# Kernel tuning notes

Hardware: AMD Instinct MI355X
Metric: run time of the kernel (lower is better)

Reference implementation:

```python
import jax, jax.numpy as jnp
import numpy as np

B = 262144
SPACE = 64
H1, H2 = 128, 64
ACTION_SCALES = np.array([32, 64, 96, 128, 160, 192, 224, 256, 16, 48, 80, 112, 144, 176, 208, 240], dtype=np.int32)
MAX_SCALE = int(ACTION_SCALES.max())  # 256


def setup_inputs() -> dict:
    key = jax.random.key(0)
    ks = jax.random.split(key, 8)
    state = jax.random.normal(ks[0], (B, SPACE), dtype=jnp.float32)
    dim_idx = jax.random.randint(ks[1], (B,), 0, len(ACTION_SCALES)).astype(jnp.float32)
    # last column carries the integer dimension index, as in the torch module
    inp = jnp.concatenate([state, dim_idx[:, None]], axis=1)  # (B, SPACE+1)
    s = 1.0 / np.sqrt(SPACE + 1)
    W1 = jax.random.uniform(ks[2], (H1, SPACE + 1), jnp.float32, -s, s)
    b1 = jnp.zeros((H1,), jnp.float32)
    s = 1.0 / np.sqrt(H1)
    W2 = jax.random.uniform(ks[3], (H2, H1), jnp.float32, -s, s)
    b2 = jnp.zeros((H2,), jnp.float32)
    s = 1.0 / np.sqrt(H2)
    W3 = jax.random.uniform(ks[4], (MAX_SCALE, H2), jnp.float32, -s, s)
    b3 = jnp.zeros((MAX_SCALE,), jnp.float32)
    scale_table = jnp.asarray(ACTION_SCALES)
    return {"input": inp, "scale_table": scale_table,
            "W1": W1, "b1": b1, "W2": W2, "b2": b2, "W3": W3, "b3": b3}


def reference(input, scale_table, W1, b1, W2, b2, W3, b3):
    dim_idx = input[:, -1].astype(jnp.int32)                 # (B,)
    x = jax.nn.relu(input @ W1.T + b1)                        # (B, 128)
    x = jax.nn.relu(x @ W2.T + b2)                            # (B, 64)
    logits = x @ W3.T + b3                                    # (B, max_scale)
    scales = scale_table[dim_idx]                             # (B,) gather replaces python loop
    mask = jnp.arange(logits.shape[-1])[None, :] < scales[:, None]  # (B, max_scale) bool
    logits = jnp.where(mask, logits, jnp.float32(-1e9))
    probs = jax.nn.softmax(logits, axis=-1)
    return probs, mask
```

## Files before the change

### kernel.cpp

```cpp
#include <hip/hip_runtime.h>
#include <hip/hip_bf16.h>

#define B_ROWS 262144
#define IN_DIM 65

typedef short short8 __attribute__((ext_vector_type(8)));
typedef float f32x4 __attribute__((ext_vector_type(4)));

static __device__ __forceinline__ short f2bf(float f) {
    union { float f; unsigned u; } v; v.f = f;
    unsigned r = v.u + 0x7fff + ((v.u >> 16) & 1);
    return (short)(r >> 16);
}
static __device__ __forceinline__ float bfbits2f(unsigned hi16) {
    union { unsigned u; float f; } v; v.u = hi16;
    return v.f;
}

__global__ void convert_weights(const float* __restrict__ W1,
                                const float* __restrict__ W2,
                                const float* __restrict__ W3,
                                short* __restrict__ ws) {
    int tid = blockIdx.x * 256 + threadIdx.x;
    if (tid < 8192) {
        int n = tid >> 6, k = tid & 63;
        ws[tid] = f2bf(W1[n * IN_DIM + k]);
    } else if (tid < 16384) {
        ws[tid] = f2bf(W2[tid - 8192]);
    } else if (tid < 32768) {
        ws[tid] = f2bf(W3[tid - 16384]);
    }
}

__global__ __launch_bounds__(256, 4) void policy_kernel(
    const float* __restrict__ inp,
    const int*   __restrict__ scale_table,
    const float* __restrict__ W1,
    const float* __restrict__ b1,
    const float* __restrict__ b2,
    const float* __restrict__ b3,
    const short* __restrict__ wbf,
    float* __restrict__ out)
{
    __shared__ __align__(16) char ldsbuf[4][4352];

    const int wave = threadIdx.x >> 6;
    const int lane = threadIdx.x & 63;
    const int l = lane & 15;
    const int q = lane >> 4;

    const int rb = blockIdx.x * 64 + wave * 16;

    short* sh = (short*)(ldsbuf[wave]);
    float* T  = (float*)(ldsbuf[wave]);

    const short* W1b = wbf;
    const short* W2b = wbf + 8192;
    const short* W3b = wbf + 16384;

    short8 a1[2];
    {
        const float* rowp = inp + (size_t)(rb + l) * IN_DIM;
        #pragma unroll
        for (int s = 0; s < 2; s++)
            #pragma unroll
            for (int j = 0; j < 8; j++)
                a1[s][j] = f2bf(rowp[s * 32 + q * 8 + j]);
    }

    float dimf[4]; int scl[4];
    #pragma unroll
    for (int r = 0; r < 4; r++) {
        dimf[r] = inp[(size_t)(rb + q * 4 + r) * IN_DIM + 64];
        scl[r]  = scale_table[(int)dimf[r]];
    }

    #pragma unroll
    for (int nt = 0; nt < 8; nt++) {
        f32x4 c = {0.f, 0.f, 0.f, 0.f};
        #pragma unroll
        for (int s = 0; s < 2; s++) {
            short8 b = *(const short8*)(W1b + (nt * 16 + l) * 64 + s * 32 + q * 8);
            c = __builtin_amdgcn_mfma_f32_16x16x32_bf16(a1[s], b, c, 0, 0, 0);
        }
        const int cidx = nt * 16 + l;
        const float w64  = W1[(size_t)cidx * IN_DIM + 64];
        const float bias = b1[cidx];
        #pragma unroll
        for (int r = 0; r < 4; r++) {
            float v = fmaxf(c[r] + dimf[r] * w64 + bias, 0.f);
            sh[(q * 4 + r) * 136 + cidx] = f2bf(v);
        }
    }

    short8 a2[4];
    #pragma unroll
    for (int s = 0; s < 4; s++)
        a2[s] = *(const short8*)(sh + l * 136 + s * 32 + q * 8);

    #pragma unroll
    for (int nt = 0; nt < 4; nt++) {
        f32x4 c = {0.f, 0.f, 0.f, 0.f};
        #pragma unroll
        for (int s = 0; s < 4; s++) {
            short8 b = *(const short8*)(W2b + (nt * 16 + l) * 128 + s * 32 + q * 8);
            c = __builtin_amdgcn_mfma_f32_16x16x32_bf16(a2[s], b, c, 0, 0, 0);
        }
        const int cidx = nt * 16 + l;
        const float bias = b2[cidx];
        #pragma unroll
        for (int r = 0; r < 4; r++) {
            float v = fmaxf(c[r] + bias, 0.f);
            sh[(q * 4 + r) * 72 + cidx] = f2bf(v);
        }
    }

    short8 a3[2];
    #pragma unroll
    for (int s = 0; s < 2; s++)
        a3[s] = *(const short8*)(sh + l * 72 + s * 32 + q * 8);

    unsigned lgp[16][2];
    #pragma unroll
    for (int nt = 0; nt < 16; nt++) {
        f32x4 c = {0.f, 0.f, 0.f, 0.f};
        #pragma unroll
        for (int s = 0; s < 2; s++) {
            short8 b = *(const short8*)(W3b + (nt * 16 + l) * 64 + s * 32 + q * 8);
            c = __builtin_amdgcn_mfma_f32_16x16x32_bf16(a3[s], b, c, 0, 0, 0);
        }
        const float bias = b3[nt * 16 + l];
        #pragma unroll
        for (int p = 0; p < 2; p++) {
            unsigned lo = (unsigned)(unsigned short)f2bf(c[p * 2 + 0] + bias);
            unsigned hi = (unsigned)(unsigned short)f2bf(c[p * 2 + 1] + bias);
            lgp[nt][p] = lo | (hi << 16);
        }
    }

    float* outP = out;
    float* outM = out + (size_t)B_ROWS * 256;

    #pragma unroll
    for (int r = 0; r < 4; r++) {
        const int sc = scl[r];

        float mx = -3.0e38f;
        #pragma unroll
        for (int nt = 0; nt < 16; nt++) {
            unsigned p = lgp[nt][r >> 1];
            float v = bfbits2f((r & 1) ? (p & 0xffff0000u) : (p << 16));
            int cc = nt * 16 + l;
            if (cc < sc) mx = fmaxf(mx, v);
        }
        #pragma unroll
        for (int off = 1; off < 16; off <<= 1)
            mx = fmaxf(mx, __shfl_xor(mx, off, 64));

        float sum = 0.f;
        #pragma unroll
        for (int nt = 0; nt < 16; nt++) {
            unsigned p = lgp[nt][r >> 1];
            float v = bfbits2f((r & 1) ? (p & 0xffff0000u) : (p << 16));
            int cc = nt * 16 + l;
            float e = (cc < sc) ? __expf(v - mx) : 0.f;
            T[q * 260 + nt * 16 + l] = e;
            sum += e;
        }
        #pragma unroll
        for (int off = 1; off < 16; off <<= 1)
            sum += __shfl_xor(sum, off, 64);

        const float inv = 1.f / sum;
        const size_t orow = (size_t)(rb + q * 4 + r);
        float* po = outP + orow * 256;
        float* mo = outM + orow * 256;
        #pragma unroll
        for (int k = 0; k < 4; k++) {
            const int c0 = k * 64 + l * 4;
            f32x4 v = *(const f32x4*)(T + q * 260 + c0);
            v[0] *= inv; v[1] *= inv; v[2] *= inv; v[3] *= inv;
            f32x4 m;
            m[0] = (c0 + 0 < sc) ? 1.f : 0.f;
            m[1] = (c0 + 1 < sc) ? 1.f : 0.f;
            m[2] = (c0 + 2 < sc) ? 1.f : 0.f;
            m[3] = (c0 + 3 < sc) ? 1.f : 0.f;
            __builtin_nontemporal_store(v, (f32x4*)(po + c0));
            __builtin_nontemporal_store(m, (f32x4*)(mo + c0));
        }
    }
}

extern "C" void kernel_launch(void* const* d_in, const int* in_sizes, int n_in,
                              void* d_out, int out_size, void* d_ws, size_t ws_size,
                              hipStream_t stream) {
    const float* inp = (const float*)d_in[0];
    const int*   st  = (const int*)  d_in[1];
    const float* W1  = (const float*)d_in[2];
    const float* b1  = (const float*)d_in[3];
    const float* W2  = (const float*)d_in[4];
    const float* b2  = (const float*)d_in[5];
    const float* W3  = (const float*)d_in[6];
    const float* b3  = (const float*)d_in[7];
    float* out = (float*)d_out;
    short* wbf = (short*)d_ws;

    convert_weights<<<128, 256, 0, stream>>>(W1, W2, W3, wbf);
    policy_kernel<<<B_ROWS / 64, 256, 0, stream>>>(inp, st, W1, b1, b2, b3, wbf, out);
}
```

Measured before the change: 670.5 us.

## Split fused MLP-softmax into logits kernel and streaming softmax kernel

The fused kernel is split in two. The first kernel runs the three-layer MFMA MLP and writes packed bf16 logit pairs into the mask output region as scratch. The second is a grid-stride softmax kernel with higher occupancy that reads those logits, applies the scale mask, and writes probabilities and mask; it also drops the max subtraction before exp. This aims to free registers and improve occupancy in the store-heavy phase. The cost is an extra round-trip of the bf16 logits through global memory, plus overflow risk if logits are ever large.

```diff
diff --git a/kernel.cpp b/kernel.cpp
--- a/kernel.cpp
+++ b/kernel.cpp
@@ -6,6 +6,7 @@
 
 typedef short short8 __attribute__((ext_vector_type(8)));
 typedef float f32x4 __attribute__((ext_vector_type(4)));
+typedef unsigned u32x4 __attribute__((ext_vector_type(4)));
 
 static __device__ __forceinline__ short f2bf(float f) {
     union { float f; unsigned u; } v; v.f = f;
@@ -32,15 +33,14 @@
     }
 }
 
-__global__ __launch_bounds__(256, 4) void policy_kernel(
+__global__ __launch_bounds__(256, 4) void mlp_logits_kernel(
     const float* __restrict__ inp,
-    const int*   __restrict__ scale_table,
     const float* __restrict__ W1,
     const float* __restrict__ b1,
     const float* __restrict__ b2,
     const float* __restrict__ b3,
     const short* __restrict__ wbf,
-    float* __restrict__ out)
+    unsigned* __restrict__ lgout)
 {
     __shared__ __align__(16) char ldsbuf[4][4352];
 
@@ -52,7 +52,6 @@
     const int rb = blockIdx.x * 64 + wave * 16;
 
     short* sh = (short*)(ldsbuf[wave]);
-    float* T  = (float*)(ldsbuf[wave]);
 
     const short* W1b = wbf;
     const short* W2b = wbf + 8192;
@@ -68,12 +67,10 @@
                 a1[s][j] = f2bf(rowp[s * 32 + q * 8 + j]);
     }
 
-    float dimf[4]; int scl[4];
-    #pragma unroll
-    for (int r = 0; r < 4; r++) {
+    float dimf[4];
+    #pragma unroll
+    for (int r = 0; r < 4; r++)
         dimf[r] = inp[(size_t)(rb + q * 4 + r) * IN_DIM + 64];
-        scl[r]  = scale_table[(int)dimf[r]];
-    }
 
     #pragma unroll
     for (int nt = 0; nt < 8; nt++) {
@@ -120,7 +117,7 @@
     for (int s = 0; s < 2; s++)
         a3[s] = *(const short8*)(sh + l * 72 + s * 32 + q * 8);
 
-    unsigned lgp[16][2];
+    unsigned* slot = lgout + (size_t)(rb >> 1) * 512 + (size_t)q * 1024;
     #pragma unroll
     for (int nt = 0; nt < 16; nt++) {
         f32x4 c = {0.f, 0.f, 0.f, 0.f};
@@ -134,60 +131,59 @@
         for (int p = 0; p < 2; p++) {
             unsigned lo = (unsigned)(unsigned short)f2bf(c[p * 2 + 0] + bias);
             unsigned hi = (unsigned)(unsigned short)f2bf(c[p * 2 + 1] + bias);
-            lgp[nt][p] = lo | (hi << 16);
-        }
-    }
-
+            slot[p * 512 + nt * 16 + l] = lo | (hi << 16);
+        }
+    }
+}
+
+__global__ __launch_bounds__(256, 8) void softmax_kernel(
+    const float* __restrict__ inp,
+    const int*   __restrict__ scale_table,
+    float* __restrict__ out)
+{
     float* outP = out;
     float* outM = out + (size_t)B_ROWS * 256;
-
-    #pragma unroll
-    for (int r = 0; r < 4; r++) {
-        const int sc = scl[r];
-
-        float mx = -3.0e38f;
-        #pragma unroll
-        for (int nt = 0; nt < 16; nt++) {
-            unsigned p = lgp[nt][r >> 1];
-            float v = bfbits2f((r & 1) ? (p & 0xffff0000u) : (p << 16));
-            int cc = nt * 16 + l;
-            if (cc < sc) mx = fmaxf(mx, v);
-        }
-        #pragma unroll
-        for (int off = 1; off < 16; off <<= 1)
-            mx = fmaxf(mx, __shfl_xor(mx, off, 64));
-
-        float sum = 0.f;
-        #pragma unroll
-        for (int nt = 0; nt < 16; nt++) {
-            unsigned p = lgp[nt][r >> 1];
-            float v = bfbits2f((r & 1) ? (p & 0xffff0000u) : (p << 16));
-            int cc = nt * 16 + l;
-            float e = (cc < sc) ? __expf(v - mx) : 0.f;
-            T[q * 260 + nt * 16 + l] = e;
-            sum += e;
-        }
-        #pragma unroll
-        for (int off = 1; off < 16; off <<= 1)
-            sum += __shfl_xor(sum, off, 64);
-
-        const float inv = 1.f / sum;
-        const size_t orow = (size_t)(rb + q * 4 + r);
-        float* po = outP + orow * 256;
-        float* mo = outM + orow * 256;
-        #pragma unroll
-        for (int k = 0; k < 4; k++) {
-            const int c0 = k * 64 + l * 4;
-            f32x4 v = *(const f32x4*)(T + q * 260 + c0);
-            v[0] *= inv; v[1] *= inv; v[2] *= inv; v[3] *= inv;
-            f32x4 m;
-            m[0] = (c0 + 0 < sc) ? 1.f : 0.f;
-            m[1] = (c0 + 1 < sc) ? 1.f : 0.f;
-            m[2] = (c0 + 2 < sc) ? 1.f : 0.f;
-            m[3] = (c0 + 3 < sc) ? 1.f : 0.f;
-            __builtin_nontemporal_store(v, (f32x4*)(po + c0));
-            __builtin_nontemporal_store(m, (f32x4*)(mo + c0));
-        }
+    const unsigned* lg = (const unsigned*)outM;
+
+    const int lane = threadIdx.x & 63;
+    const int gw = (int)((blockIdx.x * blockDim.x + threadIdx.x) >> 6);
+    const int nw = (int)((gridDim.x * blockDim.x) >> 6);
+
+    for (int m = gw; m < B_ROWS / 2; m += nw) {
+        u32x4 pk = *(const u32x4*)(lg + (size_t)m * 512 + lane * 4);
+
+        const int r0 = 2 * m, r1 = 2 * m + 1;
+        const int sc0 = scale_table[(int)inp[(size_t)r0 * IN_DIM + 64]];
+        const int sc1 = scale_table[(int)inp[(size_t)r1 * IN_DIM + 64]];
+        const bool v0 = (lane * 4) < sc0;
+        const bool v1 = (lane * 4) < sc1;
+
+        float e0[4], e1[4];
+        float s0 = 0.f, s1 = 0.f;
+        #pragma unroll
+        for (int j = 0; j < 4; j++) {
+            e0[j] = v0 ? __expf(bfbits2f(pk[j] << 16)) : 0.f;
+            e1[j] = v1 ? __expf(bfbits2f(pk[j] & 0xffff0000u)) : 0.f;
+            s0 += e0[j]; s1 += e1[j];
+        }
+        #pragma unroll
+        for (int off = 1; off < 64; off <<= 1) {
+            s0 += __shfl_xor(s0, off, 64);
+            s1 += __shfl_xor(s1, off, 64);
+        }
+        const float i0 = 1.f / s0, i1 = 1.f / s1;
+        const float f0 = v0 ? 1.f : 0.f, f1 = v1 ? 1.f : 0.f;
+
+        f32x4 p0, p1, mk0, mk1;
+        #pragma unroll
+        for (int j = 0; j < 4; j++) {
+            p0[j] = e0[j] * i0; p1[j] = e1[j] * i1;
+            mk0[j] = f0;        mk1[j] = f1;
+        }
+        __builtin_nontemporal_store(p0,  (f32x4*)(outP + (size_t)r0 * 256 + lane * 4));
+        __builtin_nontemporal_store(p1,  (f32x4*)(outP + (size_t)r1 * 256 + lane * 4));
+        __builtin_nontemporal_store(mk0, (f32x4*)(outM + (size_t)r0 * 256 + lane * 4));
+        __builtin_nontemporal_store(mk1, (f32x4*)(outM + (size_t)r1 * 256 + lane * 4));
     }
 }
 
@@ -204,7 +200,9 @@
     const float* b3  = (const float*)d_in[7];
     float* out = (float*)d_out;
     short* wbf = (short*)d_ws;
+    unsigned* lgout = (unsigned*)(out + (size_t)B_ROWS * 256);
 
     convert_weights<<<128, 256, 0, stream>>>(W1, W2, W3, wbf);
-    policy_kernel<<<B_ROWS / 64, 256, 0, stream>>>(inp, st, W1, b1, b2, b3, wbf, out);
-}
+    mlp_logits_kernel<<<B_ROWS / 64, 256, 0, stream>>>(inp, W1, b1, b2, b3, wbf, lgout);
+    softmax_kernel<<<2048, 256, 0, stream>>>(inp, st, out);
+}
```

New measurement: 692.8 us. 1.03x slower.
